# Performance work log

Hardware: AMD Instinct MI355X
Metric: run time of the kernel (lower is better)

Reference implementation:

```python
import jax, jax.numpy as jnp
import numpy as np

SEARCH_RANGE = 4  # matches args.search_range


def _displacements(r):
    # Exact channel ordering of the original double loop:
    # I=0 -> (0,0); then for i=1..r: (-i,0),(+i,0),(0,-i),(0,+i),
    # then for j=1..r: (-i,-j),(+i,+j),(-i,+j),(+i,-j).
    ds = [(0, 0)]
    for i in range(1, r + 1):
        ds += [(-i, 0), (i, 0), (0, -i), (0, i)]
        for j in range(1, r + 1):
            ds += [(-i, -j), (i, j), (-i, j), (i, -j)]
    return ds


def setup_inputs() -> dict:
    key = jax.random.key(0)
    k1, k2 = jax.random.split(key)
    B, C, H, W = 4, 128, 96, 160
    src = jax.random.normal(k1, (B, C, H, W), dtype=jnp.float32)
    tgt = jax.random.normal(k2, (B, C, H, W), dtype=jnp.float32)
    return {"src": src, "tgt": tgt}


def reference(src, tgt):
    r = SEARCH_RANGE
    B, C, H, W = src.shape
    D = (2 * r + 1) ** 2  # 81 displacement channels
    # Zero-pad tgt spatially so out-of-range shifted regions contribute 0,
    # matching the torch version's zero-initialized output slices.
    tgt_pad = jnp.pad(tgt, ((0, 0), (0, 0), (r, r), (r, r)))
    chans = []
    for dy, dx in _displacements(r):
        # shifted[b,c,y,x] = tgt[b,c,y+dy,x+dx] (0 outside)
        t = jax.lax.dynamic_slice(tgt_pad, (0, 0, r + dy, r + dx), (B, C, H, W))
        chans.append(jnp.einsum('bchw,bchw->bhw', src, t))
    out = jnp.stack(chans, axis=1)  # [B, D, H, W]
    return out / D
```

## Files before the change

kernel.cpp:

```cpp
#include <hip/hip_runtime.h>
#include <hip/hip_bf16.h>

#define BATCH 4
#define CHAN 128
#define HGT 96
#define WID 160
#define HW (HGT * WID)
#define THREADS 512
#define TENSOR_ELEMS (BATCH * CHAN * HGT * WID)
#define WS_NEED ((size_t)(2 * (size_t)TENSOR_ELEMS * 2))

typedef __attribute__((ext_vector_type(8))) short short8;
typedef __attribute__((ext_vector_type(4))) float float4v;

__device__ __forceinline__ int chan_of(int dy, int dx) {
    if (dy == 0 && dx == 0) return 0;
    if (dx == 0) { int i = dy < 0 ? -dy : dy; return 1 + (i - 1) * 20 + (dy < 0 ? 0 : 1); }
    if (dy == 0) { int i = dx < 0 ? -dx : dx; return 1 + (i - 1) * 20 + (dx < 0 ? 2 : 3); }
    int i = dy < 0 ? -dy : dy;
    int j = dx < 0 ? -dx : dx;
    int s = (dy < 0) ? (dx < 0 ? 0 : 2) : (dx < 0 ? 3 : 1);
    return 1 + (i - 1) * 20 + 4 + (j - 1) * 4 + s;
}

__device__ __forceinline__ unsigned pk2(float a, float b) {
    __hip_bfloat162 h = __float22bfloat162_rn(make_float2(a, b));
    unsigned u;
    __builtin_memcpy(&u, &h, 4);
    return u;
}

union sl_u { uint4 v; short8 s; };

__global__ __launch_bounds__(256)
void nhwc_bf16_kernel(const float* __restrict__ src,
                      const float* __restrict__ tgt,
                      ushort* __restrict__ ws) {
    __shared__ unsigned s_t[64][65];
    int r = blockIdx.x;
    const int xb = r % 3; r /= 3;
    const int y  = r % HGT; r /= HGT;
    const int b  = r % BATCH; r /= BATCH;
    const float* in = r ? tgt : src;
    ushort* op0 = ws + (size_t)r * TENSOR_ELEMS;
    const int x0 = xb * 64;
    const int npx = (x0 + 64 <= WID) ? 64 : (WID - x0);

    const int t  = threadIdx.x;
    const int x1 = t & 63, cp0 = t >> 6;
    if (x1 < npx) {
        const int base = (b * CHAN * HGT + y) * WID + x0 + x1;
        #pragma unroll
        for (int i = 0; i < 16; ++i) {
            const int cp = cp0 + i * 4;
            s_t[cp][x1] = pk2(in[base + (2 * cp) * HW],
                              in[base + (2 * cp + 1) * HW]);
        }
    }
    __syncthreads();
    const int x2 = t >> 2, g = t & 3;
    if (x2 < npx) {
        ushort* op = op0 + ((size_t)(b * HGT + y) * WID + x0 + x2) * CHAN + g * 32;
        #pragma unroll
        for (int k = 0; k < 4; ++k) {
            uint4 v;
            v.x = s_t[g * 16 + k * 4 + 0][x2];
            v.y = s_t[g * 16 + k * 4 + 1][x2];
            v.z = s_t[g * 16 + k * 4 + 2][x2];
            v.w = s_t[g * 16 + k * 4 + 3][x2];
            *(uint4*)(op + k * 8) = v;
        }
    }
}

__global__ __launch_bounds__(THREADS, 4)
void cost_volume_mfma(const ushort* __restrict__ srcT,
                      const ushort* __restrict__ tgtT,
                      float* __restrict__ out) {
    __shared__ __align__(16) uint4 s_b[4736];
    __shared__ int s_tab[81];

    const int tid  = threadIdx.x;
    const int wv   = tid >> 6;
    const int wvy  = wv & 3;
    const int wvd  = wv >> 2;
    const int lane = tid & 63;
    const int q    = lane >> 4;
    const int ln   = lane & 15;

    const int w    = blockIdx.x;
    const int slab = w & 7;
    const int b    = slab >> 1;
    const int yh   = slab & 1;
    const int t    = w >> 3;
    const int x0   = (t % 10) * 16;
    const int y0   = yh * 48 + (t / 10) * 4;

    if (tid < 81) s_tab[tid] = chan_of(tid / 9 - 4, tid % 9 - 4) * HW;

    const ushort* tbase = tgtT + (size_t)b * HGT * WID * CHAN;
    #pragma unroll
    for (int k = 0; k < 9; ++k) {
        const int u   = k * THREADS + tid;
        const int j   = u & 15;
        const int v16 = u >> 4;
        const int row = v16 / 24;
        const int x   = v16 - row * 24;
        const int gr  = y0 - 4 + row;
        const int gx  = x0 - 4 + x;
        const int oct = j ^ (x & 15);
        unsigned* lp = (unsigned*)&s_b[k * THREADS + (tid & ~63)];
        if (((unsigned)gr < (unsigned)HGT) && ((unsigned)gx < (unsigned)WID)) {
            const unsigned* gp =
                (const unsigned*)(tbase + ((gr * WID + gx) * CHAN + oct * 8));
            __builtin_amdgcn_global_load_lds(gp, lp, 16, 0, 0);
        } else {
            s_b[u] = make_uint4(0u, 0u, 0u, 0u);
        }
    }

    const int y = y0 + wvy;
    const ushort* abase =
        srcT + ((size_t)(b * HGT + y) * WID + x0 + ln) * CHAN + q * 8;
    short8 afr[4];
    #pragma unroll
    for (int ks = 0; ks < 4; ++ks)
        afr[ks] = *(const short8*)(abase + ks * 32);

    __syncthreads();

    float4v aa0[5], aa1[5];
    #define COMPUTE_DY(DD, DYI)                                               \
        {                                                                     \
            const int rr = wvy + (DYI);                                       \
            float4v a0 = (float4v){0.f, 0.f, 0.f, 0.f};                       \
            float4v a1 = (float4v){0.f, 0.f, 0.f, 0.f};                       \
            _Pragma("unroll")                                                 \
            for (int ks = 0; ks < 4; ++ks) {                                  \
                sl_u b0;                                    \
                b0.v = s_b[(rr * 24 + ln) * 16 + ((q + ks * 4) ^ ln)];        \
                a0 = __builtin_amdgcn_mfma_f32_16x16x32_bf16(afr[ks], b0.s, a0, 0, 0, 0); \
            }                                                                 \
            _Pragma("unroll")                                                 \
            for (int ks = 0; ks < 4; ++ks) {                                  \
                sl_u b1;                                 \
                b1.v = s_b[(rr * 24 + 16 + ln) * 16 + ((q + ks * 4) ^ ln)];   \
                a1 = __builtin_amdgcn_mfma_f32_16x16x32_bf16(afr[ks], b1.s, a1, 0, 0, 0); \
            }                                                                 \
            aa0[DD] = a0; aa1[DD] = a1;                                       \
        }
    if (wvd == 0) {
        #pragma unroll
        for (int dd = 0; dd < 4; ++dd) COMPUTE_DY(dd, dd)
    } else {
        #pragma unroll
        for (int dd = 0; dd < 5; ++dd) COMPUTE_DY(dd, dd + 4)
    }

    __syncthreads();

    float* s_o = (float*)s_b;
    const float inv = 1.0f / 81.0f;
    #define EPI_DY(DD, DYI)                                                   \
        _Pragma("unroll")                                                     \
        for (int reg = 0; reg < 4; ++reg) {                                   \
            const int m = q * 4 + reg;                                        \
            const int t0x = ln - m;                        \
            if ((unsigned)t0x <= 8u)                                          \
                s_o[((DYI) * 9 + t0x) * 68 + wvy * 16 + m] = aa0[DD][reg] * inv; \
            const int t1x = ln + 16 - m;                   \
            if ((unsigned)t1x <= 8u)                                          \
                s_o[((DYI) * 9 + t1x) * 68 + wvy * 16 + m] = aa1[DD][reg] * inv; \
        }
    if (wvd == 0) {
        #pragma unroll
        for (int dd = 0; dd < 4; ++dd) EPI_DY(dd, dd)
    } else {
        #pragma unroll
        for (int dd = 0; dd < 5; ++dd) EPI_DY(dd, dd + 4)
    }
    __syncthreads();

    const size_t ob = (size_t)b * 81 * HW + (size_t)y0 * WID + x0;
    #pragma unroll
    for (int it = 0; it < 3; ++it) {
        const int v = it * THREADS + tid;
        if (v < 1296) {
            const int xq  = v & 3;
            const int row = v >> 2;
            const int cix = row >> 2;
            const int yy  = row & 3;
            float4v val = *(const float4v*)&s_o[cix * 68 + yy * 16 + xq * 4];
            *(float4v*)&out[ob + s_tab[cix] + yy * WID + xq * 4] = val;
        }
    }
}

#define FST_DECODE(TAG, U)                                                    \
    const int u##TAG   = (U);                                                 \
    const int xq##TAG  = u##TAG % 6;                                          \
    const int r6##TAG  = u##TAG / 6;                                          \
    const int oct##TAG = r6##TAG & 15;                                        \
    const int row##TAG = r6##TAG >> 4;                                        \
    const int gr##TAG  = y0 - 4 + row##TAG;                                   \
    const int gx##TAG  = x0 - 4 + xq##TAG * 4;                                \
    const bool ok##TAG = ((unsigned)gr##TAG < (unsigned)HGT) &&               \
                         ((unsigned)gx##TAG < (unsigned)WID);                 \
    const int ga##TAG  = tb + (oct##TAG * 8 * HGT + gr##TAG) * WID + gx##TAG;

#define FST_ISSUE(TAG, COND)                                                  \
    _Pragma("unroll")                                                         \
    for (int j = 0; j < 8; ++j)                                               \
        p##TAG[j] = (COND) ? *(const float4v*)(tgt + ga##TAG + j * HW)        \
                           : (float4v){0.f, 0.f, 0.f, 0.f};

#define FST_WRITE(TAG)                                                        \
    _Pragma("unroll")                                                         \
    for (int i = 0; i < 4; ++i) {                                             \
        const int xl = xq##TAG * 4 + i;                                       \
        uint4 val;                                                            \
        val.x = pk2(p##TAG[0][i], p##TAG[1][i]);                              \
        val.y = pk2(p##TAG[2][i], p##TAG[3][i]);                              \
        val.z = pk2(p##TAG[4][i], p##TAG[5][i]);                              \
        val.w = pk2(p##TAG[6][i], p##TAG[7][i]);                              \
        s_b[(row##TAG * 24 + xl) * 16 + (oct##TAG ^ (xl & 15))] = val;        \
    }

__global__ __launch_bounds__(THREADS, 4)
void cost_volume_fused(const float* __restrict__ src,
                       const float* __restrict__ tgt,
                       float* __restrict__ out) {
    __shared__ __align__(16) uint4 s_b[4736];
    __shared__ int s_tab[81];

    const int tid  = threadIdx.x;
    const int wv   = tid >> 6;
    const int wvy  = wv & 3;
    const int wvd  = wv >> 2;
    const int lane = tid & 63;
    const int q    = lane >> 4;
    const int ln   = lane & 15;

    const int w    = blockIdx.x;
    const int slab = w & 7;
    const int b    = slab >> 1;
    const int yh   = slab & 1;
    const int t    = w >> 3;
    const int x0   = (t % 10) * 16;
    const int y0   = yh * 48 + (t / 10) * 4;

    if (tid < 81) s_tab[tid] = chan_of(tid / 9 - 4, tid % 9 - 4) * HW;

    const int tb = b * CHAN * HGT * WID;

    FST_DECODE(0, tid)
    FST_DECODE(1, tid + 512)
    FST_DECODE(2, tid + 1024)
    const bool has2 = tid < 128;

    float4v p0[8], p1[8], p2[8];
    FST_ISSUE(0, ok0)

    const int y = y0 + wvy;
    const int sbase = (b * CHAN * HGT + y) * WID + x0 + ln + q * 8 * HW;
    float apay[32];
    #pragma unroll
    for (int ks = 0; ks < 4; ++ks)
        #pragma unroll
        for (int j = 0; j < 8; ++j)
            apay[ks * 8 + j] = src[sbase + (ks * 32 + j) * HW];

    FST_ISSUE(1, ok1)
    FST_WRITE(0)
    FST_ISSUE(2, has2 && ok2)
    short8 afr[4];
    #pragma unroll
    for (int ks = 0; ks < 4; ++ks) {
        sl_u f;
        f.v.x = pk2(apay[ks * 8 + 0], apay[ks * 8 + 1]);
        f.v.y = pk2(apay[ks * 8 + 2], apay[ks * 8 + 3]);
        f.v.z = pk2(apay[ks * 8 + 4], apay[ks * 8 + 5]);
        f.v.w = pk2(apay[ks * 8 + 6], apay[ks * 8 + 7]);
        afr[ks] = f.s;
    }
    FST_WRITE(1)
    if (has2) { FST_WRITE(2) }

    __syncthreads();

    float4v aa0[5], aa1[5];
    if (wvd == 0) {
        #pragma unroll
        for (int dd = 0; dd < 4; ++dd) COMPUTE_DY(dd, dd)
    } else {
        #pragma unroll
        for (int dd = 0; dd < 5; ++dd) COMPUTE_DY(dd, dd + 4)
    }

    __syncthreads();

    float* s_o = (float*)s_b;
    const float inv = 1.0f / 81.0f;
    if (wvd == 0) {
        #pragma unroll
        for (int dd = 0; dd < 4; ++dd) EPI_DY(dd, dd)
    } else {
        #pragma unroll
        for (int dd = 0; dd < 5; ++dd) EPI_DY(dd, dd + 4)
    }
    __syncthreads();

    const size_t ob = (size_t)b * 81 * HW + (size_t)y0 * WID + x0;
    #pragma unroll
    for (int it = 0; it < 3; ++it) {
        const int v = it * THREADS + tid;
        if (v < 1296) {
            const int xq  = v & 3;
            const int row = v >> 2;
            const int cix = row >> 2;
            const int yy  = row & 3;
            float4v val = *(const float4v*)&s_o[cix * 68 + yy * 16 + xq * 4];
            *(float4v*)&out[ob + s_tab[cix] + yy * WID + xq * 4] = val;
        }
    }
}

extern "C" void kernel_launch(void* const* d_in, const int* in_sizes, int n_in,
                              void* d_out, int out_size, void* d_ws, size_t ws_size,
                              hipStream_t stream) {
    const float* src = (const float*)d_in[0];
    const float* tgt = (const float*)d_in[1];
    float* out = (float*)d_out;
    if (d_ws && ws_size >= WS_NEED) {
        ushort* ws = (ushort*)d_ws;
        nhwc_bf16_kernel<<<dim3(2304, 1, 1), dim3(256, 1, 1), 0, stream>>>(src, tgt, ws);
        cost_volume_mfma<<<dim3(960, 1, 1), dim3(THREADS, 1, 1), 0, stream>>>(
            ws, ws + TENSOR_ELEMS, out);
    } else {
        cost_volume_fused<<<dim3(960, 1, 1), dim3(THREADS, 1, 1), 0, stream>>>(src, tgt, out);
    }
}
```

Before: 119.1 us.

## Convert src to bf16 inside MFMA kernel instead of separate NHWC pass

The pre-pass now transposes and converts only tgt to NHWC bf16. The cost-volume kernel reads src directly from the fp32 NCHW layout and packs it into bf16 A fragments in registers. This drops the write and re-read of a full bf16 src copy and halves the work of the transpose kernel. In exchange the main kernel does strided fp32 loads (8 per fragment, stride HW) that are coalesced only across 16 lanes, and it issues them before the tgt LDS loads.

```diff
diff --git a/kernel.cpp b/kernel.cpp
--- a/kernel.cpp
+++ b/kernel.cpp
@@ -8,7 +8,7 @@
 #define HW (HGT * WID)
 #define THREADS 512
 #define TENSOR_ELEMS (BATCH * CHAN * HGT * WID)
-#define WS_NEED ((size_t)(2 * (size_t)TENSOR_ELEMS * 2))
+#define WS_NEED ((size_t)TENSOR_ELEMS * 2)
 
 typedef __attribute__((ext_vector_type(8))) short short8;
 typedef __attribute__((ext_vector_type(4))) float float4v;
@@ -33,16 +33,12 @@
 union sl_u { uint4 v; short8 s; };
 
 __global__ __launch_bounds__(256)
-void nhwc_bf16_kernel(const float* __restrict__ src,
-                      const float* __restrict__ tgt,
-                      ushort* __restrict__ ws) {
+void nhwc_bf16_tgt(const float* __restrict__ tgt, ushort* __restrict__ ws) {
     __shared__ unsigned s_t[64][65];
     int r = blockIdx.x;
     const int xb = r % 3; r /= 3;
     const int y  = r % HGT; r /= HGT;
-    const int b  = r % BATCH; r /= BATCH;
-    const float* in = r ? tgt : src;
-    ushort* op0 = ws + (size_t)r * TENSOR_ELEMS;
+    const int b  = r;
     const int x0 = xb * 64;
     const int npx = (x0 + 64 <= WID) ? 64 : (WID - x0);
 
@@ -53,14 +49,14 @@
         #pragma unroll
         for (int i = 0; i < 16; ++i) {
             const int cp = cp0 + i * 4;
-            s_t[cp][x1] = pk2(in[base + (2 * cp) * HW],
-                              in[base + (2 * cp + 1) * HW]);
+            s_t[cp][x1] = pk2(tgt[base + (2 * cp) * HW],
+                              tgt[base + (2 * cp + 1) * HW]);
         }
     }
     __syncthreads();
     const int x2 = t >> 2, g = t & 3;
     if (x2 < npx) {
-        ushort* op = op0 + ((size_t)(b * HGT + y) * WID + x0 + x2) * CHAN + g * 32;
+        ushort* op = ws + ((size_t)(b * HGT + y) * WID + x0 + x2) * CHAN + g * 32;
         #pragma unroll
         for (int k = 0; k < 4; ++k) {
             uint4 v;
@@ -74,7 +70,7 @@
 }
 
 __global__ __launch_bounds__(THREADS, 4)
-void cost_volume_mfma(const ushort* __restrict__ srcT,
+void cost_volume_mfma(const float* __restrict__ src,
                       const ushort* __restrict__ tgtT,
                       float* __restrict__ out) {
     __shared__ __align__(16) uint4 s_b[4736];
@@ -97,6 +93,34 @@
     const int y0   = yh * 48 + (t / 10) * 4;
 
     if (tid < 81) s_tab[tid] = chan_of(tid / 9 - 4, tid % 9 - 4) * HW;
+
+    const int y = y0 + wvy;
+    const int sbase = (b * CHAN * HGT + y) * WID + x0 + ln + q * 8 * HW;
+    short8 afr[4];
+    {
+        float c0[8], c1[8];
+        #define LOADA(BUF, KS)                                                \
+            _Pragma("unroll")                                                 \
+            for (int j = 0; j < 8; ++j)                                       \
+                BUF[j] = src[sbase + ((KS) * 32 + j) * HW];
+        #define CVTA(DST, BUF)                                                \
+            {                                                                 \
+                sl_u f;                                                       \
+                f.v.x = pk2(BUF[0], BUF[1]);                                  \
+                f.v.y = pk2(BUF[2], BUF[3]);                                  \
+                f.v.z = pk2(BUF[4], BUF[5]);                                  \
+                f.v.w = pk2(BUF[6], BUF[7]);                                  \
+                DST = f.s;                                                    \
+            }
+        LOADA(c0, 0)
+        LOADA(c1, 1)
+        CVTA(afr[0], c0)
+        LOADA(c0, 2)
+        CVTA(afr[1], c1)
+        LOADA(c1, 3)
+        CVTA(afr[2], c0)
+        CVTA(afr[3], c1)
+    }
 
     const ushort* tbase = tgtT + (size_t)b * HGT * WID * CHAN;
     #pragma unroll
@@ -118,14 +142,6 @@
             s_b[u] = make_uint4(0u, 0u, 0u, 0u);
         }
     }
-
-    const int y = y0 + wvy;
-    const ushort* abase =
-        srcT + ((size_t)(b * HGT + y) * WID + x0 + ln) * CHAN + q * 8;
-    short8 afr[4];
-    #pragma unroll
-    for (int ks = 0; ks < 4; ++ks)
-        afr[ks] = *(const short8*)(abase + ks * 32);
 
     __syncthreads();
 
@@ -333,9 +349,8 @@
     float* out = (float*)d_out;
     if (d_ws && ws_size >= WS_NEED) {
         ushort* ws = (ushort*)d_ws;
-        nhwc_bf16_kernel<<<dim3(2304, 1, 1), dim3(256, 1, 1), 0, stream>>>(src, tgt, ws);
-        cost_volume_mfma<<<dim3(960, 1, 1), dim3(THREADS, 1, 1), 0, stream>>>(
-            ws, ws + TENSOR_ELEMS, out);
+        nhwc_bf16_tgt<<<dim3(1152, 1, 1), dim3(256, 1, 1), 0, stream>>>(tgt, ws);
+        cost_volume_mfma<<<dim3(960, 1, 1), dim3(THREADS, 1, 1), 0, stream>>>(src, ws, out);
     } else {
         cost_volume_fused<<<dim3(960, 1, 1), dim3(THREADS, 1, 1), 0, stream>>>(src, tgt, out);
     }
```

Result: no change. 117.2 us (-1.6%).
